# Performance work log

Measured on AMD Instinct MI355X. Metric: run time of the kernel, lower is better.

Reference implementation:

```python
import jax, jax.numpy as jnp
import numpy as np

B, S, H, NH = 2, 2048, 768, 12
D = H // NH            # head dim = 64
R = 256                # relative-position buckets (Embedding(256, D))
MAX_REL = 128


def _rel_indices(s):
    # indices[i, j] = clip(j - i, -MAX_REL, MAX_REL - 1) + MAX_REL  in [0, R)
    pos = np.arange(s)
    rel = pos[None, :] - pos[:, None]
    return jnp.asarray(np.clip(rel, -MAX_REL, MAX_REL - 1) + MAX_REL, dtype=jnp.int32)


def setup_inputs() -> dict:
    key = jax.random.key(0)
    ks = jax.random.split(key, 8)
    sc = 0.02
    return {
        "hidden_states": jax.random.normal(ks[0], (B, S, H), jnp.float32),
        "input_mask": jnp.ones((B, S), jnp.float32),
        "Wq": jax.random.normal(ks[1], (H, H), jnp.float32) * sc,
        "bq": jnp.zeros((H,), jnp.float32),
        "Wk": jax.random.normal(ks[2], (H, H), jnp.float32) * sc,
        "bk": jnp.zeros((H,), jnp.float32),
        "Wv": jax.random.normal(ks[3], (H, H), jnp.float32) * sc,
        "bv": jnp.zeros((H,), jnp.float32),
        "rel_key_emb": jax.random.normal(ks[4], (R, D), jnp.float32) * sc,
        "rel_value_emb": jax.random.normal(ks[5], (R, D), jnp.float32) * sc,
        "indices": _rel_indices(S),
    }


def _heads(x):
    # [B, S, H] -> [B, NH, S, D]
    return x.reshape(B, S, NH, D).transpose(0, 2, 1, 3)


def reference(hidden_states, input_mask, Wq, bq, Wk, bk, Wv, bv,
              rel_key_emb, rel_value_emb, indices):
    q = _heads(hidden_states @ Wq + bq)
    k = _heads(hidden_states @ Wk + bk)
    v = _heads(hidden_states @ Wv + bv)

    scale = 1.0 / jnp.sqrt(jnp.asarray(D, hidden_states.dtype))
    scores = jnp.einsum("bhid,bhjd->bhij", q, k) * scale  # [B,NH,S,S]

    # relative position key bias: gather along bucket axis per (i, j)
    rel_scores = jnp.einsum("bhid,rd->bhir", q, rel_key_emb) * scale  # [B,NH,S,R]
    idx = jnp.broadcast_to(indices[None, None], scores.shape)         # [B,NH,S,S]
    scores = scores + jnp.take_along_axis(rel_scores, idx, axis=3)

    mask_bias = (1.0 - input_mask)[:, None, None, :] * -10000.0
    probs = jax.nn.softmax(scores + mask_bias, axis=-1)               # [B,NH,S,S]

    ctx = jnp.einsum("bhij,bhjd->bhid", probs, v)                     # [B,NH,S,D]

    # scatter-add attention probs into relative buckets, then matmul values
    rows = jnp.arange(S)[:, None]  # broadcast with indices [S,S]
    rel_probs = jnp.zeros_like(rel_scores).at[:, :, rows, indices].add(probs)
    ctx = ctx + jnp.einsum("bhir,rd->bhid", rel_probs, rel_value_emb)

    return ctx.transpose(0, 2, 1, 3).reshape(B, S, H)
```

## Files before the change

kernel.cpp:

```cpp
#include <hip/hip_runtime.h>
#include <hip/hip_bf16.h>
#include <math.h>


#define LDS_ATOMIC_ADD(p, v) __hip_atomic_fetch_add((p), (v), __ATOMIC_RELAXED, __HIP_MEMORY_SCOPE_WORKGROUP)

typedef short short8v __attribute__((ext_vector_type(8)));
typedef short short4v __attribute__((ext_vector_type(4)));
typedef float f32x4 __attribute__((ext_vector_type(4)));

#define MFMA16x16x32(a, b, c) __builtin_amdgcn_mfma_f32_16x16x32_bf16((a), (b), (c), 0, 0, 0)

__device__ inline short f2bf(float f) {
  unsigned u = __float_as_uint(f);
  unsigned r = (u + 0x7FFFu + ((u >> 16) & 1u)) >> 16;
  return (short)r;
}
__device__ inline float bf2f(short b) {
  return __uint_as_float(((unsigned)(unsigned short)b) << 16);
}

__global__ __launch_bounds__(256) void prep_hs_kernel(
    const float* __restrict__ hs, short* __restrict__ hi, short* __restrict__ lo) {
  const size_t base = ((size_t)blockIdx.x * 256 + threadIdx.x) * 8;
  const float4 a = *(const float4*)&hs[base];
  const float4 b = *(const float4*)&hs[base + 4];
  float x[8] = {a.x, a.y, a.z, a.w, b.x, b.y, b.z, b.w};
  short8v h, l;
  #pragma unroll
  for (int i = 0; i < 8; ++i) {
    h[i] = f2bf(x[i]);
    l[i] = f2bf(x[i] - bf2f(h[i]));
  }
  *(short8v*)&hi[base] = h;
  *(short8v*)&lo[base] = l;
}

__global__ __launch_bounds__(256) void prep_wt_kernel(
    const float* __restrict__ Wq, const float* __restrict__ Wk,
    const float* __restrict__ Wv, short* __restrict__ wt) {
  __shared__ float tile[64][65];
  const int t = threadIdx.x, tx = t & 15, ty = t >> 4;
  const int w = blockIdx.z;
  const float* W = (w == 0) ? Wq : (w == 1) ? Wk : Wv;
  const int k0 = blockIdx.x * 64, n0 = blockIdx.y * 64;
  #pragma unroll
  for (int rr = 0; rr < 4; ++rr) {
    const int kr = rr * 16 + ty;
    const float4 v = *(const float4*)&W[(size_t)(k0 + kr) * 768 + n0 + tx * 4];
    tile[kr][tx*4 + 0] = v.x; tile[kr][tx*4 + 1] = v.y;
    tile[kr][tx*4 + 2] = v.z; tile[kr][tx*4 + 3] = v.w;
  }
  __syncthreads();
  #pragma unroll
  for (int rr = 0; rr < 4; ++rr) {
    const int nr = rr * 16 + ty;
    short4v s;
    #pragma unroll
    for (int c = 0; c < 4; ++c) s[c] = f2bf(tile[tx*4 + c][nr]);
    *(short4v*)&wt[((size_t)w * 768 + n0 + nr) * 768 + k0 + tx * 4] = s;
  }
}

__global__ __launch_bounds__(256) void rvet_kernel(
    const float* __restrict__ rve, const float* __restrict__ rke,
    short* __restrict__ rvet, short* __restrict__ rkeb) {
  const int t = threadIdx.x;
  #pragma unroll 4
  for (int e = 0; e < 64; ++e) {
    const int idx = e*256 + t;
    const int r = idx >> 6, d = idx & 63;
    rvet[d*256 + r] = f2bf(rve[idx]);
    rkeb[idx]       = f2bf(rke[idx]);
  }
}

__global__ __launch_bounds__(256) void qkv_mfma_kernel(
    const short* __restrict__ hs_hi, const short* __restrict__ hs_lo,
    const short* __restrict__ wt,
    const float* __restrict__ bq, const float* __restrict__ bk,
    const float* __restrict__ bv,
    short* __restrict__ qbf, short* __restrict__ kbf, short* __restrict__ vtbf) {
  __shared__ short lds[3 * 8192];
  short* Ah = lds;
  short* Al = lds + 8192;
  short* Bt = lds + 16384;

  const int t = threadIdx.x, lane = t & 63, wv = t >> 6;
  const int wm = wv & 1, wn = wv >> 1;
  const int lrow = lane & 15, g = lane >> 4;
  const int m0 = blockIdx.x * 128, n0 = blockIdx.y * 128, w = blockIdx.z;
  const short* Bg = wt + (size_t)w * 768 * 768;
  const float* bias = (w == 0) ? bq : (w == 1) ? bk : bv;

  int srow[4], sc[4];
  #pragma unroll
  for (int e = 0; e < 4; ++e) {
    const int id = t + 256*e;
    srow[e] = id >> 3; sc[e] = id & 7;
  }

  #pragma unroll
  for (int e = 0; e < 4; ++e) {
    const int row = srow[e], c = sc[e];
    const int dst = row*64 + ((c ^ (row & 7)) * 8);
    *(short8v*)&Ah[dst] = *(const short8v*)&hs_hi[(size_t)(m0 + row)*768 + c*8];
    *(short8v*)&Al[dst] = *(const short8v*)&hs_lo[(size_t)(m0 + row)*768 + c*8];
    *(short8v*)&Bt[dst] = *(const short8v*)&Bg[(size_t)(n0 + row)*768 + c*8];
  }
  __syncthreads();

  f32x4 acc[4][4] = {};

  for (int kt = 0; kt < 12; ++kt) {
    short8v pa[4], pl[4], pb[4];
    const bool have_next = (kt < 11);
    if (have_next) {
      const int k0n = (kt + 1) * 64;
      #pragma unroll
      for (int e = 0; e < 4; ++e) {
        const int row = srow[e], c = sc[e];
        pa[e] = *(const short8v*)&hs_hi[(size_t)(m0 + row)*768 + k0n + c*8];
        pl[e] = *(const short8v*)&hs_lo[(size_t)(m0 + row)*768 + k0n + c*8];
        pb[e] = *(const short8v*)&Bg   [(size_t)(n0 + row)*768 + k0n + c*8];
      }
    }

    #pragma unroll
    for (int kc = 0; kc < 2; ++kc) {
      short8v af[4], alf[4], bfv[4];
      #pragma unroll
      for (int fm = 0; fm < 4; ++fm) {
        const int row = wm*64 + fm*16 + lrow;
        const int off = row*64 + (((kc*4 + g) ^ (row & 7)) * 8);
        af[fm]  = *(const short8v*)&Ah[off];
        alf[fm] = *(const short8v*)&Al[off];
      }
      #pragma unroll
      for (int fn = 0; fn < 4; ++fn) {
        const int row = wn*64 + fn*16 + lrow;
        bfv[fn] = *(const short8v*)&Bt[row*64 + (((kc*4 + g) ^ (row & 7)) * 8)];
      }
      #pragma unroll
      for (int fm = 0; fm < 4; ++fm)
        #pragma unroll
        for (int fn = 0; fn < 4; ++fn) {
          acc[fm][fn] = MFMA16x16x32(af[fm],  bfv[fn], acc[fm][fn]);
          acc[fm][fn] = MFMA16x16x32(alf[fm], bfv[fn], acc[fm][fn]);
        }
    }
    __syncthreads();
    if (have_next) {
      #pragma unroll
      for (int e = 0; e < 4; ++e) {
        const int row = srow[e], c = sc[e];
        const int dst = row*64 + ((c ^ (row & 7)) * 8);
        *(short8v*)&Ah[dst] = pa[e];
        *(short8v*)&Al[dst] = pl[e];
        *(short8v*)&Bt[dst] = pb[e];
      }
    }
    __syncthreads();
  }

  float bias_v[4];
  #pragma unroll
  for (int fn = 0; fn < 4; ++fn) bias_v[fn] = bias[n0 + wn*64 + fn*16 + lrow];

  #pragma unroll
  for (int fm = 0; fm < 4; ++fm) {
    #pragma unroll
    for (int r = 0; r < 4; ++r) {
      const int m = m0 + wm*64 + fm*16 + g*4 + r;
      const int b = m >> 11, s = m & 2047;
      #pragma unroll
      for (int fn = 0; fn < 4; ++fn) {
        const int n = n0 + wn*64 + fn*16 + lrow;
        const int h = n >> 6, d = n & 63;
        const size_t bh = (size_t)b*12 + h;
        const short sv = f2bf(acc[fm][fn][r] + bias_v[fn]);
        if (w == 0)      qbf [(bh*2048 + s)*64 + d] = sv;
        else if (w == 1) kbf [(bh*2048 + s)*64 + d] = sv;
        else             vtbf[(bh*64 + d)*2048 + s] = sv;
      }
    }
  }
}

__global__ __launch_bounds__(256) void rel_scores_mfma_kernel(
    const short* __restrict__ qbf, const short* __restrict__ rkeb,
    float* __restrict__ rs) {
  __shared__ short Atile[256 * 64];
  __shared__ short Btile[64 * 64];
  const int t = threadIdx.x, lane = t & 63, wv = t >> 6;
  const int lrow = lane & 15, g = lane >> 4;
  const int m0 = blockIdx.x * 256, n0 = blockIdx.y * 64;

  #pragma unroll
  for (int e = 0; e < 8; ++e) {
    const int id = t + 256*e, row = id >> 3, c = id & 7;
    *(short8v*)&Atile[row*64 + ((c ^ (row & 7)) * 8)] =
        *(const short8v*)&qbf[(size_t)(m0 + row)*64 + c*8];
  }
  #pragma unroll
  for (int e = 0; e < 2; ++e) {
    const int id = t + 256*e, row = id >> 3, c = id & 7;
    *(short8v*)&Btile[row*64 + ((c ^ (row & 7)) * 8)] =
        *(const short8v*)&rkeb[(size_t)(n0 + row)*64 + c*8];
  }
  __syncthreads();

  f32x4 acc[4][4] = {};
  #pragma unroll
  for (int kc = 0; kc < 2; ++kc) {
    short8v af[4], bfv[4];
    #pragma unroll
    for (int fm = 0; fm < 4; ++fm) {
      const int row = wv*64 + fm*16 + lrow;
      af[fm] = *(const short8v*)&Atile[row*64 + (((kc*4 + g) ^ (row & 7)) * 8)];
    }
    #pragma unroll
    for (int fn = 0; fn < 4; ++fn) {
      const int row = fn*16 + lrow;
      bfv[fn] = *(const short8v*)&Btile[row*64 + (((kc*4 + g) ^ (row & 7)) * 8)];
    }
    #pragma unroll
    for (int fm = 0; fm < 4; ++fm)
      #pragma unroll
      for (int fn = 0; fn < 4; ++fn)
        acc[fm][fn] = MFMA16x16x32(af[fm], bfv[fn], acc[fm][fn]);
  }

  #pragma unroll
  for (int fm = 0; fm < 4; ++fm)
    #pragma unroll
    for (int r = 0; r < 4; ++r) {
      const int m = m0 + wv*64 + fm*16 + g*4 + r;
      #pragma unroll
      for (int fn = 0; fn < 4; ++fn)
        rs[(size_t)m*256 + n0 + fn*16 + lrow] = acc[fm][fn][r] * 0.125f;
    }
}

__global__ __launch_bounds__(256) void attn_mfma_kernel(
    const short* __restrict__ qbf, const short* __restrict__ kbf,
    const short* __restrict__ vtbf, const float* __restrict__ rs,
    const short* __restrict__ rvet, const float* __restrict__ mask,
    float* __restrict__ out) {
  __shared__ __align__(16) char smem[37248];
  short* rp_bf  = (short*)smem;
  short* k_lds  = (short*)(smem + 16384);
  short* vt_lds = (short*)(smem + 24576);
  short* qp_lds = (short*)(smem + 32768);
  float* l_s    = (float*)(smem + 36864);
  float* edge_f = (float*)(smem + 36992);

  const int t    = threadIdx.x;
  const int lane = t & 63, wv = t >> 6;
  const int ih   = wv & 1, jh = wv >> 1;
  const int lrow = lane & 15, g = lane >> 4;
  const int swz  = (lrow & 7) << 3;

  const int bh = blockIdx.y, b = bh / 12, h = bh % 12;
  const int i0 = blockIdx.x * 32;

  const short* qb  = qbf  + ((size_t)bh*2048 + i0)*64;
  const short* kb  = kbf  + (size_t)bh*2048*64;
  const short* vtb = vtbf + (size_t)bh*64*2048;
  const float* rsb = rs   + ((size_t)bh*2048 + i0)*256;
  const float* mb  = mask + (size_t)b*2048;

  {
    const short8v z8 = {0,0,0,0,0,0,0,0};
    #pragma unroll
    for (int e = 0; e < 4; ++e) *(short8v*)&rp_bf[(e*256 + t)*8] = z8;
    if (t < 32) { l_s[t] = 0.f; edge_f[2*t] = 0.f; edge_f[2*t+1] = 0.f; }
  }
  {
    const int row = t >> 3, c = t & 7;
    *(short8v*)&qp_lds[row*64 + ((c ^ (row & 7))*8)] =
        *(const short8v*)&qb[row*64 + c*8];
  }
  #pragma unroll
  for (int e = 0; e < 2; ++e) {
    const int id = t + 256*e, row = id >> 3, c = id & 7;
    *(short8v*)&k_lds[row*64 + ((c ^ (row & 7))*8)] =
        *(const short8v*)&kb[(size_t)row*64 + c*8];
    *(short8v*)&vt_lds[row*64 + ((c ^ (row & 7))*8)] =
        *(const short8v*)&vtb[(size_t)row*2048 + c*8];
  }
  __syncthreads();

  const short8v aq0 = *(const short8v*)&qp_lds[(ih*16 + lrow)*64 + ((g*8) ^ swz)];
  const short8v aq1 = *(const short8v*)&qp_lds[(ih*16 + lrow)*64 + ((32 + g*8) ^ swz)];
  __syncthreads();

  float rs_lo[4], rs_hi[4];
  #pragma unroll
  for (int r = 0; r < 4; ++r) {
    const int il = ih*16 + 4*g + r;
    rs_lo[r] = rsb[il*256 + 0];
    rs_hi[r] = rsb[il*256 + 255];
  }
  float ls_p[4]  = {0,0,0,0};
  float rpl_p[4] = {0,0,0,0};
  float rph_p[4] = {0,0,0,0};
  f32x4 ctx0 = {0,0,0,0}, ctx1 = {0,0,0,0};

  const int srow0 = t >> 3, sc = t & 7, srow1 = (t >> 3) + 32;
  short8v stk0, stk1, stv0, stv1;

  for (int jt = 0; jt < 32; ++jt) {
    const int j0 = jt * 64;
    const bool have_next = (jt < 31);

    if (jt > 0) {
      *(short8v*)&vt_lds[srow0*64 + ((sc ^ (srow0 & 7))*8)] = stv0;
      *(short8v*)&vt_lds[srow1*64 + ((sc ^ (srow1 & 7))*8)] = stv1;
    }
    if (have_next) {
      const int j0n = j0 + 64;
      stk0 = *(const short8v*)&kb[(size_t)(j0n + srow0)*64 + sc*8];
      stk1 = *(const short8v*)&kb[(size_t)(j0n + srow1)*64 + sc*8];
      stv0 = *(const short8v*)&vtb[(size_t)srow0*2048 + j0n + sc*8];
      stv1 = *(const short8v*)&vtb[(size_t)srow1*2048 + j0n + sc*8];
    }

    f32x4 c0 = {0,0,0,0}, c1 = {0,0,0,0};
    {
      const int jr0 = jh*32 + lrow, jr1 = jh*32 + 16 + lrow;
      const short8v b00 = *(const short8v*)&k_lds[jr0*64 + ((g*8) ^ swz)];
      const short8v b01 = *(const short8v*)&k_lds[jr0*64 + ((32 + g*8) ^ swz)];
      const short8v b10 = *(const short8v*)&k_lds[jr1*64 + ((g*8) ^ swz)];
      const short8v b11 = *(const short8v*)&k_lds[jr1*64 + ((32 + g*8) ^ swz)];
      c0 = MFMA16x16x32(aq0, b00, c0);
      c0 = MFMA16x16x32(aq1, b01, c0);
      c1 = MFMA16x16x32(aq0, b10, c1);
      c1 = MFMA16x16x32(aq1, b11, c1);
    }

    const float m0v = (1.0f - mb[j0 + jh*32 + lrow])      * -10000.0f;
    const float m1v = (1.0f - mb[j0 + jh*32 + 16 + lrow]) * -10000.0f;

    if (j0 <= i0 - 192) {
      #pragma unroll
      for (int r = 0; r < 4; ++r) {
        const int il  = ih*16 + 4*g + r;
        const int wsw = ((4*g + r) & 7) << 3;
        const float p0 = __expf(c0[r]*0.125f + rs_lo[r] + m0v - 8.0f);
        const float p1 = __expf(c1[r]*0.125f + rs_lo[r] + m1v - 8.0f);
        qp_lds[il*64 + ((jh*32 + lrow) ^ wsw)]      = f2bf(p0);
        qp_lds[il*64 + ((jh*32 + 16 + lrow) ^ wsw)] = f2bf(p1);
        rpl_p[r] += p0 + p1; ls_p[r] += p0 + p1;
      }
    } else if (j0 >= i0 + 159) {
      #pragma unroll
      for (int r = 0; r < 4; ++r) {
        const int il  = ih*16 + 4*g + r;
        const int wsw = ((4*g + r) & 7) << 3;
        const float p0 = __expf(c0[r]*0.125f + rs_hi[r] + m0v - 8.0f);
        const float p1 = __expf(c1[r]*0.125f + rs_hi[r] + m1v - 8.0f);
        qp_lds[il*64 + ((jh*32 + lrow) ^ wsw)]      = f2bf(p0);
        qp_lds[il*64 + ((jh*32 + 16 + lrow) ^ wsw)] = f2bf(p1);
        rph_p[r] += p0 + p1; ls_p[r] += p0 + p1;
      }
    } else {
      #pragma unroll
      for (int r = 0; r < 4; ++r) {
        const int il  = ih*16 + 4*g + r;
        const int gi  = i0 + il;
        const int wsw = ((4*g + r) & 7) << 3;
        {
          const int jl = jh*32 + lrow, gj = j0 + jl;
          int rel = gj - gi; rel = rel < -128 ? -128 : (rel > 127 ? 127 : rel);
          const int bk = rel + 128;
          const float p = __expf(c0[r]*0.125f + rsb[il*256 + bk] + m0v - 8.0f);
          qp_lds[il*64 + (jl ^ wsw)] = f2bf(p);
          if (bk == 0)        rpl_p[r] += p;
          else if (bk == 255) rph_p[r] += p;
          else rp_bf[il*256 + (((bk >> 3) ^ (il & 7)) << 3) + (bk & 7)] = f2bf(p);
          ls_p[r] += p;
        }
        {
          const int jl = jh*32 + 16 + lrow, gj = j0 + jl;
          int rel = gj - gi; rel = rel < -128 ? -128 : (rel > 127 ? 127 : rel);
          const int bk = rel + 128;
          const float p = __expf(c1[r]*0.125f + rsb[il*256 + bk] + m1v - 8.0f);
          qp_lds[il*64 + (jl ^ wsw)] = f2bf(p);
          if (bk == 0)        rpl_p[r] += p;
          else if (bk == 255) rph_p[r] += p;
          else rp_bf[il*256 + (((bk >> 3) ^ (il & 7)) << 3) + (bk & 7)] = f2bf(p);
          ls_p[r] += p;
        }
      }
    }
    __syncthreads();

    if (have_next) {
      *(short8v*)&k_lds[srow0*64 + ((sc ^ (srow0 & 7))*8)] = stk0;
      *(short8v*)&k_lds[srow1*64 + ((sc ^ (srow1 & 7))*8)] = stk1;
    }

    {
      const int prow = ih*16 + lrow;
      const short8v pa0 = *(const short8v*)&qp_lds[prow*64 + ((g*8) ^ swz)];
      const short8v pa1 = *(const short8v*)&qp_lds[prow*64 + ((32 + g*8) ^ swz)];
      const int d0 = jh*32 + lrow, d1 = jh*32 + 16 + lrow;
      const short8v vb00 = *(const short8v*)&vt_lds[d0*64 + ((g*8) ^ swz)];
      const short8v vb01 = *(const short8v*)&vt_lds[d0*64 + ((32 + g*8) ^ swz)];
      const short8v vb10 = *(const short8v*)&vt_lds[d1*64 + ((g*8) ^ swz)];
      const short8v vb11 = *(const short8v*)&vt_lds[d1*64 + ((32 + g*8) ^ swz)];
      ctx0 = MFMA16x16x32(pa0, vb00, ctx0);
      ctx0 = MFMA16x16x32(pa1, vb01, ctx0);
      ctx1 = MFMA16x16x32(pa0, vb10, ctx1);
      ctx1 = MFMA16x16x32(pa1, vb11, ctx1);
    }
    __syncthreads();
  }

  #pragma unroll
  for (int r = 0; r < 4; ++r) {
    float a = ls_p[r], bl = rpl_p[r], bhv = rph_p[r];
    #pragma unroll
    for (int m = 1; m < 16; m <<= 1) {
      a   += __shfl_xor(a, m);
      bl  += __shfl_xor(bl, m);
      bhv += __shfl_xor(bhv, m);
    }
    if (lrow == 0) {
      const int il = ih*16 + 4*g + r;
      LDS_ATOMIC_ADD(&l_s[il], a);
      LDS_ATOMIC_ADD(&edge_f[2*il + 0], bl);
      LDS_ATOMIC_ADD(&edge_f[2*il + 1], bhv);
    }
  }
  __syncthreads();

  if (t < 32) {
    const int row = t;
    rp_bf[row*256 + (((0  ^ (row & 7))) << 3) + 0] = f2bf(edge_f[2*row + 0]);
    rp_bf[row*256 + (((31 ^ (row & 7))) << 3) + 7] = f2bf(edge_f[2*row + 1]);
  }
  __syncthreads();

  {
    const int arow = ih*16 + lrow;
    const int d0 = jh*32 + lrow, d1 = jh*32 + 16 + lrow;
    #pragma unroll
    for (int ks = 0; ks < 8; ++ks) {
      const short8v a  = *(const short8v*)&rp_bf[arow*256 + (((ks*4 + g) ^ (lrow & 7))*8)];
      const short8v b0 = *(const short8v*)&rvet[d0*256 + ks*32 + g*8];
      const short8v b1 = *(const short8v*)&rvet[d1*256 + ks*32 + g*8];
      ctx0 = MFMA16x16x32(a, b0, ctx0);
      ctx1 = MFMA16x16x32(a, b1, ctx1);
    }
  }

  #pragma unroll
  for (int r = 0; r < 4; ++r) {
    const int il = ih*16 + 4*g + r;
    const float invl = 1.0f / l_s[il];
    const int gi = i0 + il;
    out[(size_t)(b*2048 + gi)*768 + h*64 + jh*32 + lrow]      = ctx0[r] * invl;
    out[(size_t)(b*2048 + gi)*768 + h*64 + jh*32 + 16 + lrow] = ctx1[r] * invl;
  }
}

extern "C" void kernel_launch(void* const* d_in, const int* in_sizes, int n_in,
                              void* d_out, int out_size, void* d_ws, size_t ws_size,
                              hipStream_t stream) {
  const float* hs   = (const float*)d_in[0];
  const float* mask = (const float*)d_in[1];
  const float* Wq   = (const float*)d_in[2];
  const float* bq   = (const float*)d_in[3];
  const float* Wk   = (const float*)d_in[4];
  const float* bk   = (const float*)d_in[5];
  const float* Wv   = (const float*)d_in[6];
  const float* bv   = (const float*)d_in[7];
  const float* rke  = (const float*)d_in[8];
  const float* rve  = (const float*)d_in[9];

  const size_t need_bytes = 72810496;
  if (ws_size < need_bytes) return;

  short* p     = (short*)d_ws;
  float* rsw   = (float*)d_ws;
  short* hs_hi = p;
  short* hs_lo = p + 3145728;
  short* wtb   = p + 25165824;
  short* qbf   = p + 26935296;
  short* kbf   = p + 30081024;
  short* vtbf  = p + 33226752;
  short* rvet  = p + 36372480;
  short* rkeb  = p + 36388864;
  float* out   = (float*)d_out;

  prep_hs_kernel<<<dim3(1536), dim3(256), 0, stream>>>(hs, hs_hi, hs_lo);
  prep_wt_kernel<<<dim3(12, 12, 3), dim3(256), 0, stream>>>(Wq, Wk, Wv, wtb);
  rvet_kernel<<<dim3(1), dim3(256), 0, stream>>>(rve, rke, rvet, rkeb);
  qkv_mfma_kernel<<<dim3(32, 6, 3), dim3(256), 0, stream>>>(
      hs_hi, hs_lo, wtb, bq, bk, bv, qbf, kbf, vtbf);
  rel_scores_mfma_kernel<<<dim3(192, 4), dim3(256), 0, stream>>>(qbf, rkeb, rsw);
  attn_mfma_kernel<<<dim3(64, 24), dim3(256), 0, stream>>>(
      qbf, kbf, vtbf, rsw, rvet, mask, out);
}
```

Baseline: 289.5 us.

## Store rel scores as bf16, add separate V transpose, parallelize rvet prep

Three changes. The relative-score buffer is now written and read as bf16 instead of fp32, halving its traffic between rel_scores and attention. The QKV projection writes V in row layout and a new tiled kernel transposes it, avoiding strided scattered stores in the GEMM epilogue. The rvet prep kernel now runs on 64 blocks instead of one serial block. The costs are lower precision in the positional bias and an extra kernel launch plus a V round trip.

```diff
diff --git a/kernel.cpp b/kernel.cpp
--- a/kernel.cpp
+++ b/kernel.cpp
@@ -65,14 +65,10 @@
 __global__ __launch_bounds__(256) void rvet_kernel(
     const float* __restrict__ rve, const float* __restrict__ rke,
     short* __restrict__ rvet, short* __restrict__ rkeb) {
-  const int t = threadIdx.x;
-  #pragma unroll 4
-  for (int e = 0; e < 64; ++e) {
-    const int idx = e*256 + t;
-    const int r = idx >> 6, d = idx & 63;
-    rvet[d*256 + r] = f2bf(rve[idx]);
-    rkeb[idx]       = f2bf(rke[idx]);
-  }
+  const int idx = blockIdx.x * 256 + threadIdx.x;
+  const int r = idx >> 6, d = idx & 63;
+  rvet[d*256 + r] = f2bf(rve[idx]);
+  rkeb[idx]       = f2bf(rke[idx]);
 }
 
 __global__ __launch_bounds__(256) void qkv_mfma_kernel(
@@ -80,7 +76,7 @@
     const short* __restrict__ wt,
     const float* __restrict__ bq, const float* __restrict__ bk,
     const float* __restrict__ bv,
-    short* __restrict__ qbf, short* __restrict__ kbf, short* __restrict__ vtbf) {
+    short* __restrict__ qbf, short* __restrict__ kbf, short* __restrict__ vbf) {
   __shared__ short lds[3 * 8192];
   short* Ah = lds;
   short* Al = lds + 8192;
@@ -92,6 +88,7 @@
   const int m0 = blockIdx.x * 128, n0 = blockIdx.y * 128, w = blockIdx.z;
   const short* Bg = wt + (size_t)w * 768 * 768;
   const float* bias = (w == 0) ? bq : (w == 1) ? bk : bv;
+  short* outp = (w == 0) ? qbf : (w == 1) ? kbf : vbf;
 
   int srow[4], sc[4];
   #pragma unroll
@@ -178,18 +175,39 @@
         const int n = n0 + wn*64 + fn*16 + lrow;
         const int h = n >> 6, d = n & 63;
         const size_t bh = (size_t)b*12 + h;
-        const short sv = f2bf(acc[fm][fn][r] + bias_v[fn]);
-        if (w == 0)      qbf [(bh*2048 + s)*64 + d] = sv;
-        else if (w == 1) kbf [(bh*2048 + s)*64 + d] = sv;
-        else             vtbf[(bh*64 + d)*2048 + s] = sv;
-      }
-    }
+        outp[(bh*2048 + s)*64 + d] = f2bf(acc[fm][fn][r] + bias_v[fn]);
+      }
+    }
+  }
+}
+
+__global__ __launch_bounds__(256) void transpose_v_kernel(
+    const short* __restrict__ vbf, short* __restrict__ vtbf) {
+  __shared__ short tile[64][66];
+  const int t = threadIdx.x;
+  const int bh = blockIdx.y;
+  const int s0 = blockIdx.x * 64;
+  const short* src = vbf + ((size_t)bh*2048 + s0)*64;
+  const int row = t >> 3, c = t & 7;
+  #pragma unroll
+  for (int e = 0; e < 2; ++e) {
+    const int r = row + 32*e;
+    *(short8v*)&tile[r][c*8] = *(const short8v*)&src[(size_t)r*64 + c*8];
+  }
+  __syncthreads();
+  #pragma unroll
+  for (int e = 0; e < 2; ++e) {
+    const int d = row + 32*e;
+    short8v v;
+    #pragma unroll
+    for (int k = 0; k < 8; ++k) v[k] = tile[c*8 + k][d];
+    *(short8v*)&vtbf[((size_t)bh*64 + d)*2048 + s0 + c*8] = v;
   }
 }
 
 __global__ __launch_bounds__(256) void rel_scores_mfma_kernel(
     const short* __restrict__ qbf, const short* __restrict__ rkeb,
-    float* __restrict__ rs) {
+    short* __restrict__ rs) {
   __shared__ short Atile[256 * 64];
   __shared__ short Btile[64 * 64];
   const int t = threadIdx.x, lane = t & 63, wv = t >> 6;
@@ -238,13 +256,13 @@
       const int m = m0 + wv*64 + fm*16 + g*4 + r;
       #pragma unroll
       for (int fn = 0; fn < 4; ++fn)
-        rs[(size_t)m*256 + n0 + fn*16 + lrow] = acc[fm][fn][r] * 0.125f;
+        rs[(size_t)m*256 + n0 + fn*16 + lrow] = f2bf(acc[fm][fn][r] * 0.125f);
     }
 }
 
 __global__ __launch_bounds__(256) void attn_mfma_kernel(
     const short* __restrict__ qbf, const short* __restrict__ kbf,
-    const short* __restrict__ vtbf, const float* __restrict__ rs,
+    const short* __restrict__ vtbf, const short* __restrict__ rs,
     const short* __restrict__ rvet, const float* __restrict__ mask,
     float* __restrict__ out) {
   __shared__ __align__(16) char smem[37248];
@@ -267,7 +285,7 @@
   const short* qb  = qbf  + ((size_t)bh*2048 + i0)*64;
   const short* kb  = kbf  + (size_t)bh*2048*64;
   const short* vtb = vtbf + (size_t)bh*64*2048;
-  const float* rsb = rs   + ((size_t)bh*2048 + i0)*256;
+  const short* rsb = rs   + ((size_t)bh*2048 + i0)*256;
   const float* mb  = mask + (size_t)b*2048;
 
   {
@@ -299,8 +317,8 @@
   #pragma unroll
   for (int r = 0; r < 4; ++r) {
     const int il = ih*16 + 4*g + r;
-    rs_lo[r] = rsb[il*256 + 0];
-    rs_hi[r] = rsb[il*256 + 255];
+    rs_lo[r] = bf2f(rsb[il*256 + 0]);
+    rs_hi[r] = bf2f(rsb[il*256 + 255]);
   }
   float ls_p[4]  = {0,0,0,0};
   float rpl_p[4] = {0,0,0,0};
@@ -374,7 +392,7 @@
           const int jl = jh*32 + lrow, gj = j0 + jl;
           int rel = gj - gi; rel = rel < -128 ? -128 : (rel > 127 ? 127 : rel);
           const int bk = rel + 128;
-          const float p = __expf(c0[r]*0.125f + rsb[il*256 + bk] + m0v - 8.0f);
+          const float p = __expf(c0[r]*0.125f + bf2f(rsb[il*256 + bk]) + m0v - 8.0f);
           qp_lds[il*64 + (jl ^ wsw)] = f2bf(p);
           if (bk == 0)        rpl_p[r] += p;
           else if (bk == 255) rph_p[r] += p;
@@ -385,7 +403,7 @@
           const int jl = jh*32 + 16 + lrow, gj = j0 + jl;
           int rel = gj - gi; rel = rel < -128 ? -128 : (rel > 127 ? 127 : rel);
           const int bk = rel + 128;
-          const float p = __expf(c1[r]*0.125f + rsb[il*256 + bk] + m1v - 8.0f);
+          const float p = __expf(c1[r]*0.125f + bf2f(rsb[il*256 + bk]) + m1v - 8.0f);
           qp_lds[il*64 + (jl ^ wsw)] = f2bf(p);
           if (bk == 0)        rpl_p[r] += p;
           else if (bk == 255) rph_p[r] += p;
@@ -480,26 +498,28 @@
   const float* rke  = (const float*)d_in[8];
   const float* rve  = (const float*)d_in[9];
 
-  const size_t need_bytes = 72810496;
+  const size_t need_bytes = 66519040;
   if (ws_size < need_bytes) return;
 
   short* p     = (short*)d_ws;
-  float* rsw   = (float*)d_ws;
-  short* hs_hi = p;
-  short* hs_lo = p + 3145728;
-  short* wtb   = p + 25165824;
-  short* qbf   = p + 26935296;
-  short* kbf   = p + 30081024;
-  short* vtbf  = p + 33226752;
-  short* rvet  = p + 36372480;
-  short* rkeb  = p + 36388864;
+  short* rsw   = p;
+  short* hs_hi = p + 12582912;
+  short* hs_lo = p + 15728640;
+  short* wtb   = p + 18874368;
+  short* qbf   = p + 20643840;
+  short* kbf   = p + 23789568;
+  short* vbf   = p + 26935296;
+  short* vtbf  = p + 30081024;
+  short* rvet  = p + 33226752;
+  short* rkeb  = p + 33243136;
   float* out   = (float*)d_out;
 
   prep_hs_kernel<<<dim3(1536), dim3(256), 0, stream>>>(hs, hs_hi, hs_lo);
   prep_wt_kernel<<<dim3(12, 12, 3), dim3(256), 0, stream>>>(Wq, Wk, Wv, wtb);
-  rvet_kernel<<<dim3(1), dim3(256), 0, stream>>>(rve, rke, rvet, rkeb);
+  rvet_kernel<<<dim3(64), dim3(256), 0, stream>>>(rve, rke, rvet, rkeb);
   qkv_mfma_kernel<<<dim3(32, 6, 3), dim3(256), 0, stream>>>(
-      hs_hi, hs_lo, wtb, bq, bk, bv, qbf, kbf, vtbf);
+      hs_hi, hs_lo, wtb, bq, bk, bv, qbf, kbf, vbf);
+  transpose_v_kernel<<<dim3(32, 24), dim3(256), 0, stream>>>(vbf, vtbf);
   rel_scores_mfma_kernel<<<dim3(192, 4), dim3(256), 0, stream>>>(qbf, rkeb, rsw);
   attn_mfma_kernel<<<dim3(64, 24), dim3(256), 0, stream>>>(
       qbf, kbf, vtbf, rsw, rvet, mask, out);
```

Result: faster. 262.9 us (-9.2%).
